# Optimization experiments

Measured on AMD Instinct MI355X. Metric: run time of the kernel, lower is better.

The kernel has to match this reference:

```python
import jax, jax.numpy as jnp
import numpy as np

N_USERS = 40000
N_ITEMS = 20000
D = 128
N_EDGES = 320000
LAYERS = 3
EPS = 1e-7
BATCH = 4096


def setup_inputs() -> dict:
    key = jax.random.key(0)
    k1, k2, k3, k4, k5, k6, k7 = jax.random.split(key, 7)
    user_emb = jax.random.normal(k1, (N_USERS, D), jnp.float32) * 0.02
    item_emb = jax.random.normal(k2, (N_ITEMS, D), jnp.float32) * 0.02
    adj_user = jax.random.randint(k3, (N_EDGES,), 0, N_USERS)
    adj_item = jax.random.randint(k4, (N_EDGES,), 0, N_ITEMS)
    user = jax.random.randint(k5, (BATCH,), 0, N_USERS)
    # items are 1-indexed in the original forward (pos_item - 1)
    pos_item = jax.random.randint(k6, (BATCH,), 1, N_ITEMS + 1)
    neg_item = jax.random.randint(k7, (BATCH,), 1, N_ITEMS + 1)
    return dict(user_emb=user_emb, item_emb=item_emb,
                adj_user=adj_user, adj_item=adj_item,
                user=user, pos_item=pos_item, neg_item=neg_item)


def _norm_adj(adj_user, adj_item):
    # Symmetric bipartite adjacency A over (U+I) nodes with D^-1/2 A D^-1/2 norm.
    N = N_USERS + N_ITEMS
    rows = jnp.concatenate([adj_user, adj_item + N_USERS])
    cols = jnp.concatenate([adj_item + N_USERS, adj_user])
    deg = jnp.zeros((N,), jnp.float32).at[rows].add(1.0) + EPS  # (A>0).sum(1)+eps
    dinv = deg ** -0.5
    vals = dinv[rows] * dinv[cols]  # interaction values are 1.0
    return rows, cols, vals


def _encode(user_emb, item_emb, rows, cols, vals):
    N = N_USERS + N_ITEMS
    x = jnp.concatenate([user_emb, item_emb], axis=0)  # [N, D]
    acc = x
    for _ in range(LAYERS):
        # SpMM: out[r] += v_e * x[c] for each edge e=(r,c)
        x = jax.ops.segment_sum(vals[:, None] * x[cols], rows, num_segments=N)
        acc = acc + x
    all_emb = acc / jnp.float32(LAYERS + 1)  # mean over layer outputs
    return all_emb[:N_USERS], all_emb[N_USERS:]


def reference(user_emb, item_emb, adj_user, adj_item, user, pos_item, neg_item):
    rows, cols, vals = _norm_adj(adj_user, adj_item)
    u_lat, i_lat = _encode(user_emb, item_emb, rows, cols, vals)
    tu = u_lat[user]                  # [B, D]
    pi = i_lat[pos_item - 1]          # [B, D]
    ni = i_lat[neg_item - 1]          # [B, D]
    pos_scores = jnp.sum(tu * pi, axis=-1)
    neg_scores = jnp.sum(tu * ni, axis=-1)
    # BPR loss: -mean(log sigmoid(pos - neg))
    loss = -jnp.mean(jax.nn.log_sigmoid(pos_scores - neg_scores))
    return loss
```

## Files before the change

### kernel.cpp

```cpp
#include <hip/hip_runtime.h>
#include <math.h>

#define N_USERS 40000
#define N_ITEMS 20000
#define NNODES  60000
#define D       128
#define N_EDGES 320000
#define EPS_    1e-7f
#define BATCH   4096
#define STRIDE  64
#define ZSCALE  256.0f
#define BPR_BLOCKS (BATCH / 8)
#define FILL_GRPS  320
#define FILL_BLOCKS (8 * FILL_GRPS)
#define INIT_BLOCKS (((NNODES + 1) * 16 + 255) / 256)
#define FULL_BLOCKS (NNODES * 8 / 256)


typedef float vf2 __attribute__((ext_vector_type(2)));

__device__ __forceinline__ void add_fp8x16v(vf2* a, uint4 t) {
    a[0] += __builtin_amdgcn_cvt_pk_f32_fp8(t.x, false);
    a[1] += __builtin_amdgcn_cvt_pk_f32_fp8(t.x, true);
    a[2] += __builtin_amdgcn_cvt_pk_f32_fp8(t.y, false);
    a[3] += __builtin_amdgcn_cvt_pk_f32_fp8(t.y, true);
    a[4] += __builtin_amdgcn_cvt_pk_f32_fp8(t.z, false);
    a[5] += __builtin_amdgcn_cvt_pk_f32_fp8(t.z, true);
    a[6] += __builtin_amdgcn_cvt_pk_f32_fp8(t.w, false);
    a[7] += __builtin_amdgcn_cvt_pk_f32_fp8(t.w, true);
}

__device__ __forceinline__ uint4 pack_fp8x16v(const vf2* a, float w) {
    float v[16];
    #pragma unroll
    for (int k = 0; k < 8; ++k) {
        v[2 * k]     = fminf(fmaxf(w * a[k].x, -448.0f), 448.0f);
        v[2 * k + 1] = fminf(fmaxf(w * a[k].y, -448.0f), 448.0f);
    }
    int w0 = __builtin_amdgcn_cvt_pk_fp8_f32(v[0],  v[1],  0,  false);
    w0     = __builtin_amdgcn_cvt_pk_fp8_f32(v[2],  v[3],  w0, true);
    int w1 = __builtin_amdgcn_cvt_pk_fp8_f32(v[4],  v[5],  0,  false);
    w1     = __builtin_amdgcn_cvt_pk_fp8_f32(v[6],  v[7],  w1, true);
    int w2 = __builtin_amdgcn_cvt_pk_fp8_f32(v[8],  v[9],  0,  false);
    w2     = __builtin_amdgcn_cvt_pk_fp8_f32(v[10], v[11], w2, true);
    int w3 = __builtin_amdgcn_cvt_pk_fp8_f32(v[12], v[13], 0,  false);
    w3     = __builtin_amdgcn_cvt_pk_fp8_f32(v[14], v[15], w3, true);
    uint4 o; o.x = (unsigned)w0; o.y = (unsigned)w1;
    o.z = (unsigned)w2; o.w = (unsigned)w3;
    return o;
}

__device__ __forceinline__ void gather8(const int4* __restrict__ rcv, int t,
                                        const uint4* __restrict__ z, int sub,
                                        vf2* a) {
    int4 ca = rcv[2 * t], cb = rcv[2 * t + 1];
    uint4 t0 = z[(ca.x << 3) + sub];
    uint4 t1 = z[(ca.y << 3) + sub];
    uint4 t2 = z[(ca.z << 3) + sub];
    uint4 t3 = z[(ca.w << 3) + sub];
    uint4 t4 = z[(cb.x << 3) + sub];
    uint4 t5 = z[(cb.y << 3) + sub];
    uint4 t6 = z[(cb.z << 3) + sub];
    uint4 t7 = z[(cb.w << 3) + sub];
    add_fp8x16v(a, t0); add_fp8x16v(a, t1);
    add_fp8x16v(a, t2); add_fp8x16v(a, t3);
    add_fp8x16v(a, t4); add_fp8x16v(a, t5);
    add_fp8x16v(a, t6); add_fp8x16v(a, t7);
}

__global__ void fill_ell(const int4* __restrict__ au4, const int4* __restrict__ ai4,
                         int* __restrict__ fillc, int* __restrict__ colell) {
    const int bucket = blockIdx.x & 7;
    const int grp    = blockIdx.x >> 3;
    const int NE4    = N_EDGES / 4;
    for (int i = grp * 256 + threadIdx.x; i < NE4; i += FILL_GRPS * 256) {
        int4 us = au4[i];
        int4 is = ai4[i];
        int ua[4] = { us.x, us.y, us.z, us.w };
        int ia[4] = { is.x, is.y, is.z, is.w };
        #pragma unroll
        for (int k = 0; k < 4; ++k) {
            int u    = ua[k];
            int iraw = ia[k];
            int it   = N_USERS + iraw;
            if (u / 10000 == bucket) {
                int p = atomicAdd(&fillc[u], 1);
                if (p < STRIDE) colell[(u << 6) + p] = it;
            }
            if (4 + iraw / 5000 == bucket) {
                int p = atomicAdd(&fillc[it], 1);
                if (p < STRIDE) colell[(it << 6) + p] = u;
            }
        }
    }
}

__global__ void init_z(const int* __restrict__ fillc,
                       const float4* __restrict__ ue, const float4* __restrict__ ie,
                       uint2* __restrict__ z0, uint2* __restrict__ z1,
                       uint2* __restrict__ z2, int* __restrict__ colell) {
    int i   = blockIdx.x * 256 + threadIdx.x;
    if (i >= (NNODES + 1) * 16) return;
    int row = i >> 4;
    int sub = i & 15;
    if (row == NNODES) {
        uint2 zz = make_uint2(0u, 0u);
        z0[i] = zz; z1[i] = zz; z2[i] = zz;
        return;
    }
    int e = fillc[row];
    if (sub == 0) {
        int ep = (e + 7) & ~7;
        for (int k = e; k < ep; ++k) colell[(row << 6) + k] = NNODES;
    }
    float w = rsqrtf((float)e + EPS_) * ZSCALE;
    float4 e0, e1;
    if (row < N_USERS) {
        int b4 = row * 32 + sub * 2;
        e0 = ue[b4]; e1 = ue[b4 + 1];
    } else {
        int b4 = (row - N_USERS) * 32 + sub * 2;
        e0 = ie[b4]; e1 = ie[b4 + 1];
    }
    float v[8] = { e0.x * w, e0.y * w, e0.z * w, e0.w * w,
                   e1.x * w, e1.y * w, e1.z * w, e1.w * w };
    float c[8];
    #pragma unroll
    for (int k = 0; k < 8; ++k) c[k] = fminf(fmaxf(v[k], -448.0f), 448.0f);
    int lo = __builtin_amdgcn_cvt_pk_fp8_f32(c[0], c[1], 0,  false);
    lo     = __builtin_amdgcn_cvt_pk_fp8_f32(c[2], c[3], lo, true);
    int hi = __builtin_amdgcn_cvt_pk_fp8_f32(c[4], c[5], 0,  false);
    hi     = __builtin_amdgcn_cvt_pk_fp8_f32(c[6], c[7], hi, true);
    z0[i] = make_uint2((unsigned)lo, (unsigned)hi);
}

__device__ __forceinline__ void spmm_body(const int* __restrict__ cnt,
                                          const int* __restrict__ colell,
                                          const uint4* __restrict__ z,
                                          uint4* __restrict__ znxt) {
    int tid = blockIdx.x * 256 + threadIdx.x;
    int row = tid >> 3;
    int sub = threadIdx.x & 7;
    int e = cnt[row];
    const int4* rcv = (const int4*)(colell + (row << 6));
    vf2 a[8];
    #pragma unroll
    for (int k = 0; k < 8; ++k) a[k] = (vf2)(0.0f);
    int nchunks = (e + 7) >> 3;
    for (int t = 0; t < nchunks; ++t) gather8(rcv, t, z, sub, a);
    float w = 1.0f / ((float)e + EPS_);
    znxt[(row << 3) + sub] = pack_fp8x16v(a, w);
}

__global__ void spmm_L1(const int* __restrict__ cnt, const int* __restrict__ colell,
                        const uint4* __restrict__ z, uint4* __restrict__ znxt) {
    spmm_body(cnt, colell, z, znxt);
}
__global__ void spmm_L2(const int* __restrict__ cnt, const int* __restrict__ colell,
                        const uint4* __restrict__ z, uint4* __restrict__ znxt) {
    spmm_body(cnt, colell, z, znxt);
}

__global__ void bpr_loss(const float4* __restrict__ ue, const float4* __restrict__ ie,
                         const uint4* __restrict__ z1, const uint4* __restrict__ z2,
                         const int* __restrict__ cnt, const int* __restrict__ colell,
                         const int* __restrict__ user, const int* __restrict__ pos,
                         const int* __restrict__ neg,
                         float* __restrict__ lacc, int* __restrict__ done,
                         float* __restrict__ out) {
    __shared__ float s[8];
    int wave = (blockIdx.x * 256 + threadIdx.x) >> 6;
    int lane = threadIdx.x & 63;
    int sg   = lane >> 3;
    int sub  = lane & 7;
    int half = sg >> 2;
    int sgl  = sg & 3;
    int el   = wave * 2 + half;
    int u = user[el];
    int p = N_USERS + pos[el] - 1;
    int n = N_USERS + neg[el] - 1;
    int node = (sgl == 1) ? p : (sgl == 2) ? n : u;
    float cnode = 0.0f;
    vf2 vals[8];
    #pragma unroll
    for (int k = 0; k < 8; ++k) vals[k] = (vf2)(0.0f);
    if (sgl < 3) {
        int e = cnt[node];
        cnode = (float)e;
        const float4* eb = (node < N_USERS) ? ue : ie;
        int b4 = ((node < N_USERS) ? node : node - N_USERS) * 32 + sub * 4;
        float4 e0 = eb[b4], e1 = eb[b4 + 1], e2 = eb[b4 + 2], e3 = eb[b4 + 3];
        float w0 = rsqrtf(cnode + EPS_) * ZSCALE;
        vals[0] = (vf2){w0 * e0.x, w0 * e0.y}; vals[1] = (vf2){w0 * e0.z, w0 * e0.w};
        vals[2] = (vf2){w0 * e1.x, w0 * e1.y}; vals[3] = (vf2){w0 * e1.z, w0 * e1.w};
        vals[4] = (vf2){w0 * e2.x, w0 * e2.y}; vals[5] = (vf2){w0 * e2.z, w0 * e2.w};
        vals[6] = (vf2){w0 * e3.x, w0 * e3.y}; vals[7] = (vf2){w0 * e3.z, w0 * e3.w};
        int o = (node << 3) + sub;
        add_fp8x16v(vals, z1[o]);
        add_fp8x16v(vals, z2[o]);
        const int4* rcv = (const int4*)(colell + (node << 6));
        vf2 a[8];
        #pragma unroll
        for (int k = 0; k < 8; ++k) a[k] = (vf2)(0.0f);
        int nchunks = (e + 7) >> 3;
        for (int t = 0; t < nchunks; ++t) gather8(rcv, t, z2, sub, a);
        float w2 = 1.0f / (cnode + EPS_);
        #pragma unroll
        for (int k = 0; k < 8; ++k) vals[k] += w2 * a[k];
    }
    int usrc = sub | (lane & 32);
    float dotp = 0.0f;
    #pragma unroll
    for (int k = 0; k < 8; ++k) {
        dotp += __shfl(vals[k].x, usrc) * vals[k].x;
        dotp += __shfl(vals[k].y, usrc) * vals[k].y;
    }
    dotp += __shfl_down(dotp, 4, 8);
    dotp += __shfl_down(dotp, 2, 8);
    dotp += __shfl_down(dotp, 1, 8);
    float sp = __shfl(dotp, (lane & 32) + 8);
    float sn = __shfl(dotp, (lane & 32) + 16);
    float cu = __shfl(cnode, (lane & 32) + 0);
    float cp = __shfl(cnode, (lane & 32) + 8);
    float cn = __shfl(cnode, (lane & 32) + 16);
    if ((lane & 31) == 0) {
        float du = rsqrtf(cu + EPS_), dp = rsqrtf(cp + EPS_), dn = rsqrtf(cn + EPS_);
        const float inv = 1.0f / (16.0f * ZSCALE * ZSCALE);
        float diff = (sp / (du * dp) - sn / (du * dn)) * inv;
        s[(threadIdx.x >> 6) * 2 + half] =
            fminf(diff, 0.0f) - log1pf(expf(-fabsf(diff)));
    }
    __syncthreads();
    if (threadIdx.x == 0) {
        float t = s[0] + s[1] + s[2] + s[3] + s[4] + s[5] + s[6] + s[7];
        atomicAdd(lacc, t);
        __threadfence();
        int prev = atomicAdd(done, 1);
        if (prev == BPR_BLOCKS - 1) {
            float total = atomicAdd(lacc, 0.0f);
            out[0] = -total * (1.0f / (float)BATCH);
        }
    }
}

extern "C" void kernel_launch(void* const* d_in, const int* in_sizes, int n_in,
                              void* d_out, int out_size, void* d_ws, size_t ws_size,
                              hipStream_t stream) {
    const float* ue  = (const float*)d_in[0];
    const float* ie  = (const float*)d_in[1];
    const int*   au  = (const int*)d_in[2];
    const int*   ai  = (const int*)d_in[3];
    const int*   usr = (const int*)d_in[4];
    const int*   pos = (const int*)d_in[5];
    const int*   neg = (const int*)d_in[6];
    float*       out = (float*)d_out;

    const size_t ZQ4 = (size_t)(NNODES + 1) * 8;

    uint4* z0     = (uint4*)d_ws;
    uint4* z1     = z0 + ZQ4;
    uint4* z2     = z1 + ZQ4;
    int*   fillc  = (int*)(z2 + ZQ4);
    float* lacc   = (float*)(fillc + NNODES);
    int*   done   = (int*)(lacc + 1);
    int*   colell = (int*)(lacc + 4);

    hipMemsetAsync(fillc, 0, (NNODES + 4) * sizeof(int), stream);

    fill_ell<<<FILL_BLOCKS, 256, 0, stream>>>((const int4*)au, (const int4*)ai,
                                              fillc, colell);
    init_z<<<INIT_BLOCKS, 256, 0, stream>>>(fillc, (const float4*)ue,
                                            (const float4*)ie, (uint2*)z0,
                                            (uint2*)z1, (uint2*)z2, colell);

    spmm_L1<<<FULL_BLOCKS, 256, 0, stream>>>(fillc, colell, z0, z1);
    spmm_L1<<<FULL_BLOCKS, 256, 0, stream>>>(fillc, colell, z0, z1);
    spmm_L1<<<FULL_BLOCKS, 256, 0, stream>>>(fillc, colell, z0, z1);
    spmm_L2<<<FULL_BLOCKS, 256, 0, stream>>>(fillc, colell, z1, z2);

    bpr_loss<<<BPR_BLOCKS, 256, 0, stream>>>((const float4*)ue, (const float4*)ie,
                                             z1, z2, fillc, colell,
                                             usr, pos, neg, lacc, done, out);
}
```

Measured before the change: 189.6 us.

## Drop duplicate SpMM launches, pre-shift ELL columns, pad to 4, warm embeddings in fill

Removes two redundant spmm_L1 launches that recomputed the same z1. Column indices are stored pre-multiplied by 8 so the gather skips a shift, and ELL rows are padded to multiples of 4 with a 4-wide tail gather to cut wasted loads. Extra blocks in fill_ell zero the sentinel rows and the loss accumulators, replacing part of the memset, and read the embedding tables to warm the cache before init_z. The warm-up reads add memory traffic during the atomic-heavy fill phase.

```diff
diff --git a/kernel.cpp b/kernel.cpp
--- a/kernel.cpp
+++ b/kernel.cpp
@@ -13,7 +13,10 @@
 #define BPR_BLOCKS (BATCH / 8)
 #define FILL_GRPS  320
 #define FILL_BLOCKS (8 * FILL_GRPS)
-#define INIT_BLOCKS (((NNODES + 1) * 16 + 255) / 256)
+#define WARM_BLOCKS 512
+#define U4   (N_USERS * 32)
+#define TOT4 ((N_USERS + N_ITEMS) * 32)
+#define INIT_BLOCKS (NNODES * 16 / 256)
 #define FULL_BLOCKS (NNODES * 8 / 256)
 
 
@@ -54,22 +57,62 @@
                                         const uint4* __restrict__ z, int sub,
                                         vf2* a) {
     int4 ca = rcv[2 * t], cb = rcv[2 * t + 1];
-    uint4 t0 = z[(ca.x << 3) + sub];
-    uint4 t1 = z[(ca.y << 3) + sub];
-    uint4 t2 = z[(ca.z << 3) + sub];
-    uint4 t3 = z[(ca.w << 3) + sub];
-    uint4 t4 = z[(cb.x << 3) + sub];
-    uint4 t5 = z[(cb.y << 3) + sub];
-    uint4 t6 = z[(cb.z << 3) + sub];
-    uint4 t7 = z[(cb.w << 3) + sub];
+    uint4 t0 = z[ca.x + sub];
+    uint4 t1 = z[ca.y + sub];
+    uint4 t2 = z[ca.z + sub];
+    uint4 t3 = z[ca.w + sub];
+    uint4 t4 = z[cb.x + sub];
+    uint4 t5 = z[cb.y + sub];
+    uint4 t6 = z[cb.z + sub];
+    uint4 t7 = z[cb.w + sub];
     add_fp8x16v(a, t0); add_fp8x16v(a, t1);
     add_fp8x16v(a, t2); add_fp8x16v(a, t3);
     add_fp8x16v(a, t4); add_fp8x16v(a, t5);
     add_fp8x16v(a, t6); add_fp8x16v(a, t7);
 }
 
+__device__ __forceinline__ void gather4(const int4* __restrict__ rcv, int t4,
+                                        const uint4* __restrict__ z, int sub,
+                                        vf2* a) {
+    int4 ca = rcv[t4];
+    uint4 t0 = z[ca.x + sub];
+    uint4 t1 = z[ca.y + sub];
+    uint4 t2 = z[ca.z + sub];
+    uint4 t3 = z[ca.w + sub];
+    add_fp8x16v(a, t0); add_fp8x16v(a, t1);
+    add_fp8x16v(a, t2); add_fp8x16v(a, t3);
+}
+
+__device__ __forceinline__ void gather_row(const int4* __restrict__ rcv, int e,
+                                           const uint4* __restrict__ z, int sub,
+                                           vf2* a) {
+    int n4 = (e + 3) >> 2;
+    int nf = n4 >> 1;
+    for (int t = 0; t < nf; ++t) gather8(rcv, t, z, sub, a);
+    if (n4 & 1) gather4(rcv, n4 - 1, z, sub, a);
+}
+
 __global__ void fill_ell(const int4* __restrict__ au4, const int4* __restrict__ ai4,
-                         int* __restrict__ fillc, int* __restrict__ colell) {
+                         int* __restrict__ fillc, int* __restrict__ colell,
+                         const float4* __restrict__ ue, const float4* __restrict__ ie,
+                         uint2* __restrict__ z0, uint2* __restrict__ z1,
+                         uint2* __restrict__ z2, float* __restrict__ lacc,
+                         int* __restrict__ done) {
+    if (blockIdx.x >= FILL_BLOCKS) {
+        int t = (blockIdx.x - FILL_BLOCKS) * 256 + threadIdx.x;
+        if (t < 16)       z0[NNODES * 16 + t] = make_uint2(0u, 0u);
+        else if (t < 32)  z1[NNODES * 16 + (t - 16)] = make_uint2(0u, 0u);
+        else if (t < 48)  z2[NNODES * 16 + (t - 32)] = make_uint2(0u, 0u);
+        else if (t == 48) *lacc = 0.0f;
+        else if (t == 49) *done = 0;
+        float acc = 0.0f;
+        for (int i = t; i < TOT4; i += WARM_BLOCKS * 256) {
+            float4 v = (i < U4) ? ue[i] : ie[i - U4];
+            acc += v.x + v.y + v.z + v.w;
+        }
+        asm volatile("" :: "v"(acc));
+        return;
+    }
     const int bucket = blockIdx.x & 7;
     const int grp    = blockIdx.x >> 3;
     const int NE4    = N_EDGES / 4;
@@ -85,11 +128,11 @@
             int it   = N_USERS + iraw;
             if (u / 10000 == bucket) {
                 int p = atomicAdd(&fillc[u], 1);
-                if (p < STRIDE) colell[(u << 6) + p] = it;
+                if (p < STRIDE) colell[(u << 6) + p] = it << 3;
             }
             if (4 + iraw / 5000 == bucket) {
                 int p = atomicAdd(&fillc[it], 1);
-                if (p < STRIDE) colell[(it << 6) + p] = u;
+                if (p < STRIDE) colell[(it << 6) + p] = u << 3;
             }
         }
     }
@@ -97,21 +140,14 @@
 
 __global__ void init_z(const int* __restrict__ fillc,
                        const float4* __restrict__ ue, const float4* __restrict__ ie,
-                       uint2* __restrict__ z0, uint2* __restrict__ z1,
-                       uint2* __restrict__ z2, int* __restrict__ colell) {
+                       uint2* __restrict__ z0, int* __restrict__ colell) {
     int i   = blockIdx.x * 256 + threadIdx.x;
-    if (i >= (NNODES + 1) * 16) return;
     int row = i >> 4;
     int sub = i & 15;
-    if (row == NNODES) {
-        uint2 zz = make_uint2(0u, 0u);
-        z0[i] = zz; z1[i] = zz; z2[i] = zz;
-        return;
-    }
     int e = fillc[row];
     if (sub == 0) {
-        int ep = (e + 7) & ~7;
-        for (int k = e; k < ep; ++k) colell[(row << 6) + k] = NNODES;
+        int ep = (e + 3) & ~3;
+        for (int k = e; k < ep; ++k) colell[(row << 6) + k] = NNODES << 3;
     }
     float w = rsqrtf((float)e + EPS_) * ZSCALE;
     float4 e0, e1;
@@ -146,8 +182,7 @@
     vf2 a[8];
     #pragma unroll
     for (int k = 0; k < 8; ++k) a[k] = (vf2)(0.0f);
-    int nchunks = (e + 7) >> 3;
-    for (int t = 0; t < nchunks; ++t) gather8(rcv, t, z, sub, a);
+    gather_row(rcv, e, z, sub, a);
     float w = 1.0f / ((float)e + EPS_);
     znxt[(row << 3) + sub] = pack_fp8x16v(a, w);
 }
@@ -202,8 +237,7 @@
         vf2 a[8];
         #pragma unroll
         for (int k = 0; k < 8; ++k) a[k] = (vf2)(0.0f);
-        int nchunks = (e + 7) >> 3;
-        for (int t = 0; t < nchunks; ++t) gather8(rcv, t, z2, sub, a);
+        gather_row(rcv, e, z2, sub, a);
         float w2 = 1.0f / (cnode + EPS_);
         #pragma unroll
         for (int k = 0; k < 8; ++k) vals[k] += w2 * a[k];
@@ -265,16 +299,15 @@
     int*   done   = (int*)(lacc + 1);
     int*   colell = (int*)(lacc + 4);
 
-    hipMemsetAsync(fillc, 0, (NNODES + 4) * sizeof(int), stream);
-
-    fill_ell<<<FILL_BLOCKS, 256, 0, stream>>>((const int4*)au, (const int4*)ai,
-                                              fillc, colell);
+    hipMemsetAsync(fillc, 0, NNODES * sizeof(int), stream);
+
+    fill_ell<<<FILL_BLOCKS + WARM_BLOCKS, 256, 0, stream>>>(
+        (const int4*)au, (const int4*)ai, fillc, colell,
+        (const float4*)ue, (const float4*)ie,
+        (uint2*)z0, (uint2*)z1, (uint2*)z2, lacc, done);
     init_z<<<INIT_BLOCKS, 256, 0, stream>>>(fillc, (const float4*)ue,
-                                            (const float4*)ie, (uint2*)z0,
-                                            (uint2*)z1, (uint2*)z2, colell);
-
-    spmm_L1<<<FULL_BLOCKS, 256, 0, stream>>>(fillc, colell, z0, z1);
-    spmm_L1<<<FULL_BLOCKS, 256, 0, stream>>>(fillc, colell, z0, z1);
+                                            (const float4*)ie, (uint2*)z0, colell);
+
     spmm_L1<<<FULL_BLOCKS, 256, 0, stream>>>(fillc, colell, z0, z1);
     spmm_L2<<<FULL_BLOCKS, 256, 0, stream>>>(fillc, colell, z1, z2);
 
```

Measured after the change: 169.8 us. 1.12x faster.
